# Kernel tuning notes

Hardware: AMD Instinct MI355X
Metric: run time of the kernel (lower is better)

## Reference

```python
import math
import jax, jax.numpy as jnp
import numpy as np

NUM_HEADS = 32
NUM_KV_HEADS = 8
HEAD_DIM = 128
ROPE_THETA = 10000.0


def rotate_half(x):
    x1, x2 = jnp.split(x, 2, axis=-1)
    return jnp.concatenate((-x2, x1), axis=-1)


def rope_cos_sin(seq_len, dim, dtype):
    pos = jnp.arange(seq_len, dtype=jnp.float32)[:, None]            # [S,1]
    freqs = jnp.exp(-jnp.arange(0, dim, 2, dtype=jnp.float32) * (math.log(ROPE_THETA) / dim))
    ang = pos * freqs                                                # [S,D/2]
    cos = jnp.concatenate([jnp.cos(ang), jnp.cos(ang)], axis=-1)     # [S,D]
    sin = jnp.concatenate([jnp.sin(ang), jnp.sin(ang)], axis=-1)
    # broadcast over heads: [S,1,D]
    return cos[:, None, :].astype(dtype), sin[:, None, :].astype(dtype)


def setup_inputs() -> dict:
    key = jax.random.key(0)
    k1, k2, k3, k4, k5 = jax.random.split(key, 5)
    B, S, Hd = 1, 2048, 4096
    kv_dim = NUM_KV_HEADS * HEAD_DIM
    s = 0.02
    return {
        "hidden_states": jax.random.normal(k1, (B, S, Hd), jnp.float32),
        "Wq": jax.random.normal(k2, (Hd, Hd), jnp.float32) * s,
        "Wk": jax.random.normal(k3, (kv_dim, Hd), jnp.float32) * s,
        "Wv": jax.random.normal(k4, (kv_dim, Hd), jnp.float32) * s,
        "Wo": jax.random.normal(k5, (Hd, Hd), jnp.float32) * s,
    }


def reference(hidden_states, Wq, Wk, Wv, Wo):
    B, S, _ = hidden_states.shape
    H, KV, D = NUM_HEADS, NUM_KV_HEADS, HEAD_DIM
    groups = H // KV

    q = jnp.einsum('bsh,oh->bso', hidden_states, Wq).reshape(B, S, H, D)
    k = jnp.einsum('bsh,oh->bso', hidden_states, Wk).reshape(B, S, KV, D)
    v = jnp.einsum('bsh,oh->bso', hidden_states, Wv).reshape(B, S, KV, D)

    # GQA: repeat_interleave along head dim
    k = jnp.repeat(k, groups, axis=2)   # [B,S,H,D]
    v = jnp.repeat(v, groups, axis=2)

    cos, sin = rope_cos_sin(S, D, hidden_states.dtype)  # [S,1,D]
    q = q * cos + rotate_half(q) * sin
    k = k * cos + rotate_half(k) * sin

    q = q.transpose(0, 2, 1, 3)  # [B,H,S,D]
    k = k.transpose(0, 2, 1, 3)
    v = v.transpose(0, 2, 1, 3)

    scores = jnp.einsum('bhqd,bhkd->bhqk', q, k) / math.sqrt(D)
    causal = jnp.tril(jnp.ones((S, S), dtype=bool))
    scores = jnp.where(causal, scores, jnp.asarray(-1e9, scores.dtype))
    attn = jax.nn.softmax(scores, axis=-1)

    out = jnp.einsum('bhqk,bhkd->bqhd', attn, v).reshape(B, S, H * D)
    return jnp.einsum('bso,ho->bsh', out, Wo)
```

## Files before the change

### kernel.cpp

```cpp
#include <hip/hip_runtime.h>

#define S_LEN 2048
#define HD    4096
#define NH    32
#define NKV   8
#define DH    128
#define NQKV  6144
#define QKV_STRIDE_B (NQKV * 2)

typedef __bf16 bf16_t;
typedef __bf16 bf16x8 __attribute__((ext_vector_type(8)));
typedef float  f32x4  __attribute__((ext_vector_type(4)));
typedef unsigned short ushort8v __attribute__((ext_vector_type(8)));

__device__ inline unsigned short f2bf_bits(float f) {
  unsigned int u = __builtin_bit_cast(unsigned int, f);
  unsigned int r = (u + 0x7FFFu + ((u >> 16) & 1u)) >> 16;
  return (unsigned short)r;
}
__device__ inline bf16_t f2bf(float f) {
  return __builtin_bit_cast(bf16_t, f2bf_bits(f));
}
__device__ inline float bf2f(bf16_t b) {
  unsigned int u = ((unsigned int)__builtin_bit_cast(unsigned short, b)) << 16;
  return __builtin_bit_cast(float, u);
}

__device__ inline void load_lds16(const void* g, void* l) {
  __builtin_amdgcn_global_load_lds(
      (__attribute__((address_space(1))) unsigned int*)(void*)g,
      (__attribute__((address_space(3))) unsigned int*)l, 16, 0, 0);
}

__device__ inline void store_out(float* p, float v)  { *p = v; }
__device__ inline void store_out(bf16_t* p, float v) { *p = f2bf(v); }

#define SCHED0 __builtin_amdgcn_sched_barrier(0)

__global__ void cvt_kernel(const float* __restrict__ in, bf16_t* __restrict__ out, int n8) {
  int stride = gridDim.x * blockDim.x;
  for (int i = blockIdx.x * blockDim.x + threadIdx.x; i < n8; i += stride) {
    float4 v0 = reinterpret_cast<const float4*>(in)[i * 2];
    float4 v1 = reinterpret_cast<const float4*>(in)[i * 2 + 1];
    ushort8v o;
    o[0] = f2bf_bits(v0.x); o[1] = f2bf_bits(v0.y);
    o[2] = f2bf_bits(v0.z); o[3] = f2bf_bits(v0.w);
    o[4] = f2bf_bits(v1.x); o[5] = f2bf_bits(v1.y);
    o[6] = f2bf_bits(v1.z); o[7] = f2bf_bits(v1.w);
    reinterpret_cast<ushort8v*>(out)[i] = o;
  }
}

template <typename OutT>
__global__ __launch_bounds__(256)
void gemm_bt32x2_kernel(const bf16_t* __restrict__ A, const bf16_t* __restrict__ B,
                        OutT* __restrict__ C, int M, int N, int K, int nbx) {
  __shared__ __align__(16) bf16_t lA [128 * 32];
  __shared__ __align__(16) bf16_t lB [128 * 32];
  __shared__ __align__(16) bf16_t lA2[128 * 32];
  __shared__ __align__(16) bf16_t lB2[128 * 32];
  const int t = threadIdx.x;
  const int lane = t & 63, wave = t >> 6;

  const int nwg = gridDim.x;
  const int orig = blockIdx.x;
  const int xcd = orig & 7;
  const int qq = nwg >> 3, rr = nwg & 7;
  const int base = (xcd < rr) ? xcd * (qq + 1) : rr * (qq + 1) + (xcd - rr) * qq;
  const int wgid = base + (orig >> 3);
  const int row0 = (wgid / nbx) * 128, col0 = (wgid % nbx) * 128;

  const int wm = (wave >> 1) * 64, wn = (wave & 1) * 64;

  const int rA = wave * 32 + (lane >> 2);
  const int cA = (lane & 3) * 8;
  const char* Asrc0 = (const char*)(A + (size_t)(row0 + rA) * K + cA);
  const char* Asrc1 = (const char*)(A + (size_t)(row0 + rA + 16) * K + cA);
  const char* Bsrc0 = (const char*)(B + (size_t)(col0 + rA) * K + cA);
  const char* Bsrc1 = (const char*)(B + (size_t)(col0 + rA + 16) * K + cA);
  char* lAd  = (char*)lA  + wave * 2048;
  char* lBd  = (char*)lB  + wave * 2048;
  char* lA2d = (char*)lA2 + wave * 2048;
  char* lB2d = (char*)lB2 + wave * 2048;

  f32x4 acc[4][4] = {};
  const int fr = lane & 15, fq = lane >> 4;

  for (int k0 = 0; k0 < K; k0 += 64) {
    const size_t kb = (size_t)k0 * 2;
    load_lds16(Asrc0 + kb, lAd);
    load_lds16(Asrc1 + kb, lAd + 1024);
    load_lds16(Bsrc0 + kb, lBd);
    load_lds16(Bsrc1 + kb, lBd + 1024);
    load_lds16(Asrc0 + kb + 64, lA2d);
    load_lds16(Asrc1 + kb + 64, lA2d + 1024);
    load_lds16(Bsrc0 + kb + 64, lB2d);
    load_lds16(Bsrc1 + kb + 64, lB2d + 1024);
    SCHED0;
    __syncthreads();

    {
      bf16x8 af[4], bfv[4];
#pragma unroll
      for (int mi = 0; mi < 4; mi++)
        af[mi] = *reinterpret_cast<const bf16x8*>(&lA[(wm + mi * 16 + fr) * 32 + fq * 8]);
#pragma unroll
      for (int ni = 0; ni < 4; ni++)
        bfv[ni] = *reinterpret_cast<const bf16x8*>(&lB[(wn + ni * 16 + fr) * 32 + fq * 8]);
      __builtin_amdgcn_s_setprio(1);
#pragma unroll
      for (int mi = 0; mi < 4; mi++)
#pragma unroll
        for (int ni = 0; ni < 4; ni++)
          acc[mi][ni] = __builtin_amdgcn_mfma_f32_16x16x32_bf16(af[mi], bfv[ni], acc[mi][ni], 0, 0, 0);
      __builtin_amdgcn_s_setprio(0);
    }
    {
      bf16x8 af[4], bfv[4];
#pragma unroll
      for (int mi = 0; mi < 4; mi++)
        af[mi] = *reinterpret_cast<const bf16x8*>(&lA2[(wm + mi * 16 + fr) * 32 + fq * 8]);
#pragma unroll
      for (int ni = 0; ni < 4; ni++)
        bfv[ni] = *reinterpret_cast<const bf16x8*>(&lB2[(wn + ni * 16 + fr) * 32 + fq * 8]);
      __builtin_amdgcn_s_setprio(1);
#pragma unroll
      for (int mi = 0; mi < 4; mi++)
#pragma unroll
        for (int ni = 0; ni < 4; ni++)
          acc[mi][ni] = __builtin_amdgcn_mfma_f32_16x16x32_bf16(af[mi], bfv[ni], acc[mi][ni], 0, 0, 0);
      __builtin_amdgcn_s_setprio(0);
    }
    SCHED0;
    __syncthreads();
  }

#pragma unroll
  for (int mi = 0; mi < 4; mi++) {
#pragma unroll
    for (int r = 0; r < 4; r++) {
      int row = row0 + wm + mi * 16 + fq * 4 + r;
      OutT* Cp = C + (size_t)row * N + col0 + wn + fr;
#pragma unroll
      for (int ni = 0; ni < 4; ni++) store_out(Cp + ni * 16, acc[mi][ni][r]);
    }
  }
}

__global__ void rope_kernel(bf16_t* __restrict__ x, int heads, int rstride, float scale) {
  int idx = blockIdx.x * blockDim.x + threadIdx.x;
  int i = idx & 63;
  int h = (idx >> 6) % heads;
  int s = idx / (64 * heads);
  const float NEG_LOG1E4_64 = -0.14391156f;
  float freq = __expf((float)i * NEG_LOG1E4_64);
  float ang = (float)s * freq;
  float sn, cs;
  __sincosf(ang, &sn, &cs);
  bf16_t* p = x + (size_t)s * rstride + h * DH;
  float x1 = bf2f(p[i]);
  float x2 = bf2f(p[i + 64]);
  p[i]      = f2bf((x1 * cs - x2 * sn) * scale);
  p[i + 64] = f2bf((x2 * cs + x1 * sn) * scale);
}

__global__ void transpose_kernel(const bf16_t* __restrict__ in, bf16_t* __restrict__ out,
                                 int R, int C, int in_rstride) {
  __shared__ bf16_t tile[64][65];
  int c0 = blockIdx.x * 64, r0 = blockIdx.y * 64;
  int t = threadIdx.x;
#pragma unroll
  for (int i = 0; i < 16; i++) {
    int idx = t + i * 256;
    int r = idx >> 6, c = idx & 63;
    tile[r][c] = in[(size_t)(r0 + r) * in_rstride + c0 + c];
  }
  __syncthreads();
#pragma unroll
  for (int i = 0; i < 16; i++) {
    int idx = t + i * 256;
    int r = idx >> 6, c = idx & 63;
    out[(size_t)(c0 + r) * R + r0 + c] = tile[c][r];
  }
}

__global__ __launch_bounds__(256)
void attn_kernel(const bf16_t* __restrict__ Qkv, const bf16_t* __restrict__ Vt,
                 bf16_t* __restrict__ O) {
  __shared__ __align__(16) char lK[2][64 * 256];
  __shared__ __align__(16) char lV[2][64 * 256];
  __shared__ __align__(16) bf16_t lP[4][16 * 72];

  const int t = threadIdx.x, lane = t & 63, wave = t >> 6;
  const int h = blockIdx.y, kvh = h >> 2;
  const int pid = blockIdx.x;
  const int fr = lane & 15, fq = lane >> 4;

  const int gc = wave * 4 + (lane >> 4);
  const int sS = (lane & 15) ^ (gc & 15);
  const char* KsrcB = (const char*)(Qkv + HD + (size_t)kvh * DH) +
                      (size_t)gc * QKV_STRIDE_B + sS * 16;
  const int dVc = gc * 2 + (sS >> 3);
  const char* VsrcB = (const char*)Vt + (size_t)kvh * DH * S_LEN * 2 +
                      (size_t)dVc * 4096 + (sS & 7) * 16;
  char* dKw = (char*)lK[0] + wave * 1024;
  char* dVw = (char*)lV[0] + wave * 1024;

  auto stage = [&](int buf, int kv0) {
    char* dk = dKw + buf * (64 * 256);
    char* dv = dVw + buf * (64 * 256);
    const char* ks = KsrcB + (size_t)kv0 * QKV_STRIDE_B;
    const char* vs = VsrcB + (size_t)kv0 * 2;
#pragma unroll
    for (int i = 0; i < 4; i++) {
      load_lds16(ks + i * (16 * QKV_STRIDE_B), dk + i * 4096);
      load_lds16(vs + i * (size_t)(32 * 4096), dv + i * 4096);
    }
  };

  stage(0, 0);
  int buf = 0;

  for (int pass = 0; pass < 2; pass++) {
    const int qb = pass ? pid : (31 - pid);
    const int q0 = qb * 64 + wave * 16;

    bf16x8 qf[4];
    const bf16_t* Qp = Qkv + (size_t)(q0 + fr) * NQKV + h * DH + fq * 8;
#pragma unroll
    for (int kt = 0; kt < 4; kt++)
      qf[kt] = *reinterpret_cast<const bf16x8*>(Qp + kt * 32);

    f32x4 o_acc[8] = {};
    float m_run[4] = {-1e30f, -1e30f, -1e30f, -1e30f};
    float l_run[4] = {0.f, 0.f, 0.f, 0.f};

    for (int tt = 0; tt <= qb; tt++) {
      __syncthreads();
      if (tt < qb)            stage(buf ^ 1, (tt + 1) * 64);
      else if (pass == 0)     stage(buf ^ 1, 0);

      const char* cK = lK[buf];
      const char* cV = lV[buf];
      const bool diag = (tt == qb);

      f32x4 s_acc[4] = {};
      __builtin_amdgcn_s_setprio(1);
#pragma unroll
      for (int nt = 0; nt < 4; nt++) {
        const char* rowp = cK + (nt * 16 + fr) * 256;
#pragma unroll
        for (int kt = 0; kt < 4; kt++) {
          const bf16x8 kf = *reinterpret_cast<const bf16x8*>(
              rowp + (((kt * 4 + fq) ^ fr) << 4));
          s_acc[nt] = __builtin_amdgcn_mfma_f32_16x16x32_bf16(qf[kt], kf, s_acc[nt], 0, 0, 0);
        }
      }
      __builtin_amdgcn_s_setprio(0);

      float pmax[4];
#pragma unroll
      for (int r = 0; r < 4; r++) {
        if (diag) {
          const int qrel = wave * 16 + fq * 4 + r;
#pragma unroll
          for (int nt = 0; nt < 4; nt++)
            if (nt * 16 + fr > qrel) s_acc[nt][r] = -1e30f;
        }
        float mr = fmaxf(fmaxf(s_acc[0][r], s_acc[1][r]), fmaxf(s_acc[2][r], s_acc[3][r]));
#pragma unroll
        for (int off = 1; off < 16; off <<= 1) mr = fmaxf(mr, __shfl_xor(mr, off, 16));
        pmax[r] = mr;
      }
      bool nb = (pmax[0] > m_run[0] + 8.f) || (pmax[1] > m_run[1] + 8.f) ||
                (pmax[2] > m_run[2] + 8.f) || (pmax[3] > m_run[3] + 8.f);
      if (__any(nb)) {
#pragma unroll
        for (int r = 0; r < 4; r++) {
          float mnew = fmaxf(m_run[r], pmax[r]);
          float alpha = __expf(m_run[r] - mnew);
#pragma unroll
          for (int ni = 0; ni < 8; ni++) o_acc[ni][r] *= alpha;
          l_run[r] *= alpha;
          m_run[r] = mnew;
        }
      }
      bf16_t* lPw = lP[wave];
#pragma unroll
      for (int r = 0; r < 4; r++) {
        float p0 = __expf(s_acc[0][r] - m_run[r]);
        float p1 = __expf(s_acc[1][r] - m_run[r]);
        float p2 = __expf(s_acc[2][r] - m_run[r]);
        float p3 = __expf(s_acc[3][r] - m_run[r]);
        float sr = (p0 + p1) + (p2 + p3);
#pragma unroll
        for (int off = 1; off < 16; off <<= 1) sr += __shfl_xor(sr, off, 16);
        l_run[r] += sr;
        const int row = fq * 4 + r;
        lPw[row * 72 + fr]      = f2bf(p0);
        lPw[row * 72 + 16 + fr] = f2bf(p1);
        lPw[row * 72 + 32 + fr] = f2bf(p2);
        lPw[row * 72 + 48 + fr] = f2bf(p3);
      }

#pragma unroll
      for (int kk = 0; kk < 2; kk++) {
        const bf16x8 pf = *reinterpret_cast<const bf16x8*>(lPw + fr * 72 + kk * 32 + fq * 8);
        __builtin_amdgcn_s_setprio(1);
#pragma unroll
        for (int ni = 0; ni < 8; ni++) {
          const int d = ni * 16 + fr;
          const int g = d >> 1;
          const int slot = ((d & 1) * 8 + kk * 4 + fq) ^ (g & 15);
          const bf16x8 vf = *reinterpret_cast<const bf16x8*>(cV + g * 256 + (slot << 4));
          o_acc[ni] = __builtin_amdgcn_mfma_f32_16x16x32_bf16(pf, vf, o_acc[ni], 0, 0, 0);
        }
        __builtin_amdgcn_s_setprio(0);
      }
      buf ^= 1;
    }

#pragma unroll
    for (int r = 0; r < 4; r++) {
      int qrow = q0 + fq * 4 + r;
      float inv = 1.0f / l_run[r];
      bf16_t* Op = O + ((size_t)qrow * NH + h) * DH + fr;
#pragma unroll
      for (int ni = 0; ni < 8; ni++) Op[ni * 16] = f2bf(o_acc[ni][r] * inv);
    }
  }
}

extern "C" void kernel_launch(void* const* d_in, const int* in_sizes, int n_in,
                              void* d_out, int out_size, void* d_ws, size_t ws_size,
                              hipStream_t stream) {
  const float* X  = (const float*)d_in[0];
  const float* Wq = (const float*)d_in[1];
  const float* Wk = (const float*)d_in[2];
  const float* Wv = (const float*)d_in[3];
  const float* Wo = (const float*)d_in[4];
  float* out = (float*)d_out;

  char* ws = (char*)d_ws;
  size_t off = 0;
  auto alloc = [&](size_t bytes) {
    char* p = ws + off;
    off += (bytes + 255) & ~(size_t)255;
    return p;
  };
  const size_t kvdim = (size_t)NKV * DH;
  bf16_t* Xb    = (bf16_t*)alloc((size_t)S_LEN * HD * 2);
  bf16_t* Wqkvb = (bf16_t*)alloc((size_t)NQKV * HD * 2);
  bf16_t* Wob   = (bf16_t*)alloc((size_t)HD * HD * 2);
  bf16_t* QKVb  = (bf16_t*)alloc((size_t)S_LEN * NQKV * 2);
  bf16_t* Vtb   = (bf16_t*)alloc((size_t)S_LEN * kvdim * 2);
  bf16_t* AOb   = (bf16_t*)alloc((size_t)S_LEN * HD * 2);
  (void)ws_size;

  auto cvt = [&](const float* in, bf16_t* o, size_t n) {
    int n8 = (int)(n / 8);
    int blocks = (n8 + 255) / 256;
    if (blocks > 2048) blocks = 2048;
    cvt_kernel<<<dim3(blocks), dim3(256), 0, stream>>>(in, o, n8);
  };
  cvt(X,  Xb,    (size_t)S_LEN * HD);
  cvt(Wq, Wqkvb, (size_t)HD * HD);
  cvt(Wk, Wqkvb + (size_t)HD * HD,   kvdim * HD);
  cvt(Wv, Wqkvb + (size_t)(HD + kvdim) * HD, kvdim * HD);
  cvt(Wo, Wob,   (size_t)HD * HD);

  {
    int nbx = NQKV / 128, nby = S_LEN / 128;
    gemm_bt32x2_kernel<bf16_t><<<dim3(nbx * nby), dim3(256), 0, stream>>>(
        Xb, Wqkvb, QKVb, S_LEN, NQKV, HD, nbx);
  }

  rope_kernel<<<dim3(S_LEN * NH * 64 / 256), dim3(256), 0, stream>>>(
      QKVb, NH, NQKV, 0.08838834764831845f);
  rope_kernel<<<dim3(S_LEN * NKV * 64 / 256), dim3(256), 0, stream>>>(
      QKVb + HD, NKV, NQKV, 1.0f);

  transpose_kernel<<<dim3((int)kvdim / 64, S_LEN / 64), dim3(256), 0, stream>>>(
      QKVb + HD + kvdim, Vtb, S_LEN, (int)kvdim, NQKV);

  attn_kernel<<<dim3(16, NH), dim3(256), 0, stream>>>(QKVb, Vtb, AOb);

  {
    int nbx = HD / 128, nby = S_LEN / 128;
    gemm_bt32x2_kernel<float><<<dim3(nbx * nby), dim3(256), 0, stream>>>(
        AOb, Wob, out, S_LEN, HD, HD, nbx);
  }
}
```

Before: 371.5 us.

## Double-buffer LDS tiles in bf16 GEMM to overlap global loads with MFMA

The GEMM kernel now keeps two LDS buffers per operand. It issues the global-to-LDS loads for the next K-step right after the barrier and then computes on the current buffer, so there is one barrier per iteration instead of two. This is meant to hide global memory latency behind the MFMA work. In exchange, LDS per workgroup doubles, which can lower the number of resident workgroups per CU, and the explicit sched_barrier hints are removed.

```diff
diff --git a/kernel.cpp b/kernel.cpp
--- a/kernel.cpp
+++ b/kernel.cpp
@@ -34,8 +34,6 @@
 
 __device__ inline void store_out(float* p, float v)  { *p = v; }
 __device__ inline void store_out(bf16_t* p, float v) { *p = f2bf(v); }
-
-#define SCHED0 __builtin_amdgcn_sched_barrier(0)
 
 __global__ void cvt_kernel(const float* __restrict__ in, bf16_t* __restrict__ out, int n8) {
   int stride = gridDim.x * blockDim.x;
@@ -55,10 +53,10 @@
 __global__ __launch_bounds__(256)
 void gemm_bt32x2_kernel(const bf16_t* __restrict__ A, const bf16_t* __restrict__ B,
                         OutT* __restrict__ C, int M, int N, int K, int nbx) {
-  __shared__ __align__(16) bf16_t lA [128 * 32];
-  __shared__ __align__(16) bf16_t lB [128 * 32];
-  __shared__ __align__(16) bf16_t lA2[128 * 32];
-  __shared__ __align__(16) bf16_t lB2[128 * 32];
+  __shared__ __align__(16) bf16_t lA [2][128 * 32];
+  __shared__ __align__(16) bf16_t lB [2][128 * 32];
+  __shared__ __align__(16) bf16_t lA2[2][128 * 32];
+  __shared__ __align__(16) bf16_t lB2[2][128 * 32];
   const int t = threadIdx.x;
   const int lane = t & 63, wave = t >> 6;
 
@@ -78,16 +76,16 @@
   const char* Asrc1 = (const char*)(A + (size_t)(row0 + rA + 16) * K + cA);
   const char* Bsrc0 = (const char*)(B + (size_t)(col0 + rA) * K + cA);
   const char* Bsrc1 = (const char*)(B + (size_t)(col0 + rA + 16) * K + cA);
-  char* lAd  = (char*)lA  + wave * 2048;
-  char* lBd  = (char*)lB  + wave * 2048;
-  char* lA2d = (char*)lA2 + wave * 2048;
-  char* lB2d = (char*)lB2 + wave * 2048;
-
+
+  const int fr = lane & 15, fq = lane >> 4;
   f32x4 acc[4][4] = {};
-  const int fr = lane & 15, fq = lane >> 4;
-
-  for (int k0 = 0; k0 < K; k0 += 64) {
+
+  auto stage = [&](int b, int k0) {
     const size_t kb = (size_t)k0 * 2;
+    char* lAd  = (char*)lA [b] + wave * 2048;
+    char* lBd  = (char*)lB [b] + wave * 2048;
+    char* lA2d = (char*)lA2[b] + wave * 2048;
+    char* lB2d = (char*)lB2[b] + wave * 2048;
     load_lds16(Asrc0 + kb, lAd);
     load_lds16(Asrc1 + kb, lAd + 1024);
     load_lds16(Bsrc0 + kb, lBd);
@@ -96,17 +94,22 @@
     load_lds16(Asrc1 + kb + 64, lA2d + 1024);
     load_lds16(Bsrc0 + kb + 64, lB2d);
     load_lds16(Bsrc1 + kb + 64, lB2d + 1024);
-    SCHED0;
+  };
+
+  stage(0, 0);
+  int b = 0;
+  for (int k0 = 0; k0 < K; k0 += 64) {
     __syncthreads();
+    if (k0 + 64 < K) stage(b ^ 1, k0 + 64);
 
     {
       bf16x8 af[4], bfv[4];
 #pragma unroll
       for (int mi = 0; mi < 4; mi++)
-        af[mi] = *reinterpret_cast<const bf16x8*>(&lA[(wm + mi * 16 + fr) * 32 + fq * 8]);
+        af[mi] = *reinterpret_cast<const bf16x8*>(&lA[b][(wm + mi * 16 + fr) * 32 + fq * 8]);
 #pragma unroll
       for (int ni = 0; ni < 4; ni++)
-        bfv[ni] = *reinterpret_cast<const bf16x8*>(&lB[(wn + ni * 16 + fr) * 32 + fq * 8]);
+        bfv[ni] = *reinterpret_cast<const bf16x8*>(&lB[b][(wn + ni * 16 + fr) * 32 + fq * 8]);
       __builtin_amdgcn_s_setprio(1);
 #pragma unroll
       for (int mi = 0; mi < 4; mi++)
@@ -119,10 +122,10 @@
       bf16x8 af[4], bfv[4];
 #pragma unroll
       for (int mi = 0; mi < 4; mi++)
-        af[mi] = *reinterpret_cast<const bf16x8*>(&lA2[(wm + mi * 16 + fr) * 32 + fq * 8]);
+        af[mi] = *reinterpret_cast<const bf16x8*>(&lA2[b][(wm + mi * 16 + fr) * 32 + fq * 8]);
 #pragma unroll
       for (int ni = 0; ni < 4; ni++)
-        bfv[ni] = *reinterpret_cast<const bf16x8*>(&lB2[(wn + ni * 16 + fr) * 32 + fq * 8]);
+        bfv[ni] = *reinterpret_cast<const bf16x8*>(&lB2[b][(wn + ni * 16 + fr) * 32 + fq * 8]);
       __builtin_amdgcn_s_setprio(1);
 #pragma unroll
       for (int mi = 0; mi < 4; mi++)
@@ -131,8 +134,7 @@
           acc[mi][ni] = __builtin_amdgcn_mfma_f32_16x16x32_bf16(af[mi], bfv[ni], acc[mi][ni], 0, 0, 0);
       __builtin_amdgcn_s_setprio(0);
     }
-    SCHED0;
-    __syncthreads();
+    b ^= 1;
   }
 
 #pragma unroll
```

After: 395.5 us. +6.5%, slower.
